# Kernel optimization log

Measured on AMD Instinct MI355X. Metric: run time of the kernel, lower is better.

The kernel has to match this reference:

```python
import jax, jax.numpy as jnp
import numpy as np

DIM = 640
M_SPATIAL = 100  # 10*10
BATCH = 64
EPS = 1e-5


def setup_inputs() -> dict:
    key = jax.random.key(0)
    kx, = jax.random.split(key, 1)
    x = jax.random.normal(kx, (BATCH, DIM, M_SPATIAL), dtype=jnp.float32)
    # temperature buffer: log(1 / (2 * H * W)) as in BDC.__init__
    t = jnp.log(1.0 / (2.0 * M_SPATIAL) * jnp.ones((1, 1), dtype=jnp.float32))
    return {"x": x, "t": t}


def reference(x, t):
    B, dim, M = x.shape
    # x_pow2 = x @ x^T  -> [B, dim, dim]
    x_pow2 = jnp.einsum('bim,bjm->bij', x, x)
    # I_M.bmm(x_pow2*I) broadcasts diag along rows; (x_pow2*I).bmm(I_M) along cols
    d = jnp.diagonal(x_pow2, axis1=1, axis2=2)  # [B, dim], squared norms
    dcov = d[:, :, None] + d[:, None, :] - 2.0 * x_pow2
    dcov = jnp.clip(dcov, 0.0)
    dcov = jnp.exp(t) * dcov
    dcov = jnp.sqrt(dcov + EPS)
    # double centering: dcov.bmm(I_M) = row sums broadcast, I_M.bmm(dcov) = col sums
    row_mean = jnp.sum(dcov, axis=2, keepdims=True) / dim          # [B, dim, 1]
    col_mean = jnp.sum(dcov, axis=1, keepdims=True) / dim          # [B, 1, dim]
    grand_mean = jnp.sum(dcov, axis=(1, 2), keepdims=True) / (dim * dim)
    bdc = dcov - row_mean - col_mean + grand_mean                   # [B, dim, dim]
    # Triuvec: upper triangle incl. diagonal, row-major order
    iu_r, iu_c = np.triu_indices(dim)
    return bdc[:, iu_r, iu_c]  # [B, dim*(dim+1)//2]
```

## Files before the change

### kernel.cpp

```cpp
#include <hip/hip_runtime.h>
#include <math.h>

#define BATCH 64
#define DIM   640
#define MSP   100
#define BT    128
#define NT2   5
#define NPAIR2 15
#define NBLK2 960
#define PTRI  205120
#define EPSV  1e-5f

#define WS_D 0
#define WS_S 40960
#define WS_G 81920
#define XB_OFF 327936ull

typedef __attribute__((ext_vector_type(8))) short short8;
typedef __attribute__((ext_vector_type(4))) float f32x4;

__device__ __forceinline__ short f2bf(float f) {
    union { float f; unsigned u; } x; x.f = f;
    unsigned r = x.u + 0x7fffu + ((x.u >> 16) & 1u);
    return (short)(r >> 16);
}
__device__ __forceinline__ float bf2f(short h) {
    union { unsigned u; float f; } x; x.u = ((unsigned)(unsigned short)h) << 16;
    return x.f;
}

__device__ __forceinline__ void decode_pair5(int u, int& ti, int& tj) {
    ti = 0;
    while (u >= NT2 - ti) { u -= NT2 - ti; ++ti; }
    tj = ti + u;
}

__device__ __forceinline__ void decode_block128(int bid, int& b, int& ti, int& tj) {
    const int xcd = bid & 7;
    const int idx = bid >> 3;
    b = xcd + 8 * (idx & 7);
    decode_pair5(idx >> 3, ti, tj);
}

__global__ __launch_bounds__(256) void k_prep(const float* __restrict__ x,
                                              float* __restrict__ ws) {
    short* xb = (short*)((char*)ws + XB_OFF);
    const int t = threadIdx.x;
    const int rr = t >> 4, c = t & 15;
    const int row = blockIdx.x * 16 + rr;
    const int k0 = c * 8;
    const float* src = x + (size_t)row * MSP;

    float v[8];
#pragma unroll
    for (int e = 0; e < 8; ++e) v[e] = 0.f;
    if (k0 <= 88) {
        float4 u0 = *(const float4*)(src + k0);
        float4 u1 = *(const float4*)(src + k0 + 4);
        v[0] = u0.x; v[1] = u0.y; v[2] = u0.z; v[3] = u0.w;
        v[4] = u1.x; v[5] = u1.y; v[6] = u1.z; v[7] = u1.w;
    } else if (k0 == 96) {
        float4 u0 = *(const float4*)(src + 96);
        v[0] = u0.x; v[1] = u0.y; v[2] = u0.z; v[3] = u0.w;
    }

    short8 h; float s = 0.f;
#pragma unroll
    for (int e = 0; e < 8; ++e) {
        short hb = f2bf(v[e]);
        float vr = bf2f(hb);
        s += vr * vr;
        h[e] = hb;
    }
    *(short8*)(xb + (size_t)blockIdx.x * 2048 + c * 128 + rr * 8) = h;

    s += __shfl_xor(s, 1); s += __shfl_xor(s, 2);
    s += __shfl_xor(s, 4); s += __shfl_xor(s, 8);
    if (c == 0) { ws[WS_D + row] = s; ws[WS_S + row] = 0.f; }
    if (blockIdx.x == 0 && t < BATCH) ws[WS_G + t] = 0.f;
}

__global__ __launch_bounds__(256) void k_sums(const float* __restrict__ tsc,
                                              float* __restrict__ ws) {
    __shared__ float sRow[BT];
    __shared__ float sCol[BT];

    int b, ti, tj;
    decode_block128(blockIdx.x, b, ti, tj);
    const int i0 = ti * BT, j0 = tj * BT;
    const int tid = threadIdx.x;
    const short* xb = (const short*)((const char*)ws + XB_OFF);

    if (tid < BT) { sRow[tid] = 0.f; sCol[tid] = 0.f; }

    const int wave = tid >> 6, lane = tid & 63;
    const int lm = lane & 15, lq = lane >> 4;
    const int r0 = (wave >> 1) * 64, c0 = (wave & 1) * 64;

    const short* pa = xb + (size_t)(b * 40 + ((i0 + r0) >> 4)) * 2048 + lq * 128 + lm * 8;
    const short* pb = xb + (size_t)(b * 40 + ((j0 + c0) >> 4)) * 2048 + lq * 128 + lm * 8;

    f32x4 acc[4][4] = {};
#pragma unroll
    for (int ks = 0; ks < 4; ++ks) {
        short8 af[4], bf[4];
#pragma unroll
        for (int m = 0; m < 4; ++m) af[m] = *(const short8*)(pa + m * 2048 + ks * 512);
#pragma unroll
        for (int n = 0; n < 4; ++n) bf[n] = *(const short8*)(pb + n * 2048 + ks * 512);
#pragma unroll
        for (int m = 0; m < 4; ++m)
#pragma unroll
            for (int n = 0; n < 4; ++n)
                acc[m][n] = __builtin_amdgcn_mfma_f32_16x16x32_bf16(af[m], bf[n], acc[m][n], 0, 0, 0);
    }

    const float scale = expf(tsc[0]);
    const float* dn = ws + WS_D + b * DIM;
    float dj[4];
#pragma unroll
    for (int n = 0; n < 4; ++n) dj[n] = dn[j0 + c0 + 16 * n + lm];

    float rp[4][4] = {}, cp[4] = {};
#pragma unroll
    for (int m = 0; m < 4; ++m) {
        float di_[4];
#pragma unroll
        for (int r = 0; r < 4; ++r) di_[r] = dn[i0 + r0 + 16 * m + 4 * lq + r];
#pragma unroll
        for (int n = 0; n < 4; ++n)
#pragma unroll
            for (int p = 0; p < 4; ++p) {
                float v = __builtin_amdgcn_sqrtf(
                    fmaf(scale, fmaxf(fmaf(-2.f, acc[m][n][p], di_[p] + dj[n]), 0.f), EPSV));
                rp[m][p] += v; cp[n] += v;
            }
    }

    __syncthreads();
#pragma unroll
    for (int m = 0; m < 4; ++m)
#pragma unroll
        for (int p = 0; p < 4; ++p) {
            float v = rp[m][p];
            v += __shfl_xor(v, 1); v += __shfl_xor(v, 2);
            v += __shfl_xor(v, 4); v += __shfl_xor(v, 8);
            if (lm == 0) atomicAdd(&sRow[r0 + 16 * m + 4 * lq + p], v);
        }
#pragma unroll
    for (int n = 0; n < 4; ++n) {
        float v = cp[n];
        v += __shfl_xor(v, 16); v += __shfl_xor(v, 32);
        if (lq == 0) atomicAdd(&sCol[c0 + 16 * n + lm], v);
    }
    __syncthreads();

    float* S = ws + WS_S + b * DIM;
    if (tid < BT) {
        atomicAdd(&S[i0 + tid], sRow[tid]);
        if (ti != tj) atomicAdd(&S[j0 + tid], sCol[tid]);
        float gg = sRow[tid];
        gg += __shfl_xor(gg, 1);  gg += __shfl_xor(gg, 2);  gg += __shfl_xor(gg, 4);
        gg += __shfl_xor(gg, 8);  gg += __shfl_xor(gg, 16); gg += __shfl_xor(gg, 32);
        if (lane == 0) atomicAdd(&ws[WS_G + b], (ti == tj ? 1.f : 2.f) * gg);
    }
}

__global__ __launch_bounds__(256) void k_write(const float* __restrict__ tsc,
                                               const float* __restrict__ ws,
                                               float* __restrict__ out) {
    int b, ti, tj;
    decode_block128(blockIdx.x, b, ti, tj);
    const int i0 = ti * BT, j0 = tj * BT;
    const int tid = threadIdx.x;
    const short* xb = (const short*)((const char*)ws + XB_OFF);

    const int wave = tid >> 6, lane = tid & 63;
    const int lm = lane & 15, lq = lane >> 4;
    const int wr = wave >> 1, wc = wave & 1;
    const int r0 = wr * 64, c0 = wc * 64;

    const bool diag = (ti == tj);
    if (diag && wr > wc) return;
    const bool pred = diag && (wr == wc);

    const short* pa = xb + (size_t)(b * 40 + ((i0 + r0) >> 4)) * 2048 + lq * 128 + lm * 8;
    const short* pb = xb + (size_t)(b * 40 + ((j0 + c0) >> 4)) * 2048 + lq * 128 + lm * 8;

    f32x4 acc[4][4] = {};
#pragma unroll
    for (int ks = 0; ks < 4; ++ks) {
        short8 af[4], bf[4];
#pragma unroll
        for (int m = 0; m < 4; ++m) af[m] = *(const short8*)(pa + m * 2048 + ks * 512);
#pragma unroll
        for (int n = 0; n < 4; ++n) bf[n] = *(const short8*)(pb + n * 2048 + ks * 512);
#pragma unroll
        for (int m = 0; m < 4; ++m)
#pragma unroll
            for (int n = 0; n < 4; ++n)
                acc[m][n] = __builtin_amdgcn_mfma_f32_16x16x32_bf16(af[m], bf[n], acc[m][n], 0, 0, 0);
    }

    const float scale = expf(tsc[0]);
    const float inv = 1.f / (float)DIM;
    const float gmean = ws[WS_G + b] * (inv * inv);
    const float* S  = ws + WS_S + b * DIM;
    const float* dn = ws + WS_D + b * DIM;

    float dj[4], bj[4]; int jj[4];
#pragma unroll
    for (int n = 0; n < 4; ++n) {
        int j = j0 + c0 + 16 * n + lm;
        jj[n] = j; dj[n] = dn[j]; bj[n] = -S[j] * inv;
    }

    float* outb = out + (size_t)b * PTRI;
#pragma unroll
    for (int m = 0; m < 4; ++m) {
        const int ibase = i0 + r0 + 16 * m + 4 * lq;
        float di_[4], ai_[4]; int ib_[4];
#pragma unroll
        for (int r = 0; r < 4; ++r) {
            int i = ibase + r;
            di_[r] = dn[i];
            ai_[r] = gmean - S[i] * inv;
            ib_[r] = i * DIM - (i * (i - 1)) / 2 - i;
        }
#pragma unroll
        for (int n = 0; n < 4; ++n)
#pragma unroll
            for (int p = 0; p < 4; ++p) {
                float v = __builtin_amdgcn_sqrtf(
                    fmaf(scale, fmaxf(fmaf(-2.f, acc[m][n][p], di_[p] + dj[n]), 0.f), EPSV));
                if (!pred || jj[n] >= ibase + p)
                    outb[ib_[p] + jj[n]] = v + ai_[p] + bj[n];
            }
    }
}

extern "C" void kernel_launch(void* const* d_in, const int* in_sizes, int n_in,
                              void* d_out, int out_size, void* d_ws, size_t ws_size,
                              hipStream_t stream) {
    const float* x = (const float*)d_in[0];
    const float* t = (const float*)d_in[1];
    float* out = (float*)d_out;
    float* ws  = (float*)d_ws;

    k_prep <<<dim3(BATCH * DIM / 16), 256, 0, stream>>>(x, ws);
    k_sums <<<dim3(NBLK2),            256, 0, stream>>>(t, ws);
    k_write<<<dim3(NBLK2),            256, 0, stream>>>(t, ws, out);
}
```

Measured before the change: 124.5 us.

## Fuse sums and write kernels with per-batch spin barrier, reusing MFMA results

Merges the row/column-sum kernel and the output-write kernel into one kernel. Each block keeps its Gram-tile accumulators and finishes the per-batch sums, then waits on a per-batch atomic counter until all 15 tile blocks of that batch have contributed. It then writes the centered output directly from registers, so the second bf16 GEMM pass and one kernel launch are no longer needed. The cost is spin-waiting and higher register pressure. Correctness relies on all 15 blocks of a batch being co-resident, which the launch bound of 4 blocks per CU and the block ordering are meant to guarantee.

```diff
diff --git a/kernel.cpp b/kernel.cpp
--- a/kernel.cpp
+++ b/kernel.cpp
@@ -14,7 +14,8 @@
 #define WS_D 0
 #define WS_S 40960
 #define WS_G 81920
-#define XB_OFF 327936ull
+#define WS_C 81984
+#define XB_OFF 328192ull
 
 typedef __attribute__((ext_vector_type(8))) short short8;
 typedef __attribute__((ext_vector_type(4))) float f32x4;
@@ -77,11 +78,15 @@
     s += __shfl_xor(s, 1); s += __shfl_xor(s, 2);
     s += __shfl_xor(s, 4); s += __shfl_xor(s, 8);
     if (c == 0) { ws[WS_D + row] = s; ws[WS_S + row] = 0.f; }
-    if (blockIdx.x == 0 && t < BATCH) ws[WS_G + t] = 0.f;
-}
-
-__global__ __launch_bounds__(256) void k_sums(const float* __restrict__ tsc,
-                                              float* __restrict__ ws) {
+    if (blockIdx.x == 0 && t < BATCH) {
+        ws[WS_G + t] = 0.f;
+        ((unsigned*)(ws + WS_C))[t] = 0u;
+    }
+}
+
+__global__ __launch_bounds__(256, 4) void k_main(const float* __restrict__ tsc,
+                                                 float* __restrict__ ws,
+                                                 float* __restrict__ out) {
     __shared__ float sRow[BT];
     __shared__ float sCol[BT];
 
@@ -95,7 +100,8 @@
 
     const int wave = tid >> 6, lane = tid & 63;
     const int lm = lane & 15, lq = lane >> 4;
-    const int r0 = (wave >> 1) * 64, c0 = (wave & 1) * 64;
+    const int wr = wave >> 1, wc = wave & 1;
+    const int r0 = wr * 64, c0 = wc * 64;
 
     const short* pa = xb + (size_t)(b * 40 + ((i0 + r0) >> 4)) * 2048 + lq * 128 + lm * 8;
     const short* pb = xb + (size_t)(b * 40 + ((j0 + c0) >> 4)) * 2048 + lq * 128 + lm * 8;
@@ -164,55 +170,35 @@
         gg += __shfl_xor(gg, 8);  gg += __shfl_xor(gg, 16); gg += __shfl_xor(gg, 32);
         if (lane == 0) atomicAdd(&ws[WS_G + b], (ti == tj ? 1.f : 2.f) * gg);
     }
-}
-
-__global__ __launch_bounds__(256) void k_write(const float* __restrict__ tsc,
-                                               const float* __restrict__ ws,
-                                               float* __restrict__ out) {
-    int b, ti, tj;
-    decode_block128(blockIdx.x, b, ti, tj);
-    const int i0 = ti * BT, j0 = tj * BT;
-    const int tid = threadIdx.x;
-    const short* xb = (const short*)((const char*)ws + XB_OFF);
-
-    const int wave = tid >> 6, lane = tid & 63;
-    const int lm = lane & 15, lq = lane >> 4;
-    const int wr = wave >> 1, wc = wave & 1;
-    const int r0 = wr * 64, c0 = wc * 64;
+
+    unsigned* cnt = (unsigned*)(ws + WS_C);
+    __threadfence();
+    __syncthreads();
+    if (tid == 0)
+        __hip_atomic_fetch_add(cnt + b, 1u, __ATOMIC_RELEASE,
+                               __HIP_MEMORY_SCOPE_AGENT);
+    if (tid == 0) {
+        while (__hip_atomic_load(cnt + b, __ATOMIC_ACQUIRE,
+                                 __HIP_MEMORY_SCOPE_AGENT) < (unsigned)NPAIR2)
+            __builtin_amdgcn_s_sleep(2);
+    }
+    __syncthreads();
 
     const bool diag = (ti == tj);
     if (diag && wr > wc) return;
     const bool pred = diag && (wr == wc);
 
-    const short* pa = xb + (size_t)(b * 40 + ((i0 + r0) >> 4)) * 2048 + lq * 128 + lm * 8;
-    const short* pb = xb + (size_t)(b * 40 + ((j0 + c0) >> 4)) * 2048 + lq * 128 + lm * 8;
-
-    f32x4 acc[4][4] = {};
-#pragma unroll
-    for (int ks = 0; ks < 4; ++ks) {
-        short8 af[4], bf[4];
-#pragma unroll
-        for (int m = 0; m < 4; ++m) af[m] = *(const short8*)(pa + m * 2048 + ks * 512);
-#pragma unroll
-        for (int n = 0; n < 4; ++n) bf[n] = *(const short8*)(pb + n * 2048 + ks * 512);
-#pragma unroll
-        for (int m = 0; m < 4; ++m)
-#pragma unroll
-            for (int n = 0; n < 4; ++n)
-                acc[m][n] = __builtin_amdgcn_mfma_f32_16x16x32_bf16(af[m], bf[n], acc[m][n], 0, 0, 0);
-    }
-
-    const float scale = expf(tsc[0]);
     const float inv = 1.f / (float)DIM;
-    const float gmean = ws[WS_G + b] * (inv * inv);
-    const float* S  = ws + WS_S + b * DIM;
-    const float* dn = ws + WS_D + b * DIM;
-
-    float dj[4], bj[4]; int jj[4];
+    const float gmean = __hip_atomic_load(ws + WS_G + b, __ATOMIC_RELAXED,
+                                          __HIP_MEMORY_SCOPE_AGENT) * (inv * inv);
+
+    float bj[4]; int jj[4];
 #pragma unroll
     for (int n = 0; n < 4; ++n) {
         int j = j0 + c0 + 16 * n + lm;
-        jj[n] = j; dj[n] = dn[j]; bj[n] = -S[j] * inv;
+        jj[n] = j;
+        bj[n] = -__hip_atomic_load(&S[j], __ATOMIC_RELAXED,
+                                   __HIP_MEMORY_SCOPE_AGENT) * inv;
     }
 
     float* outb = out + (size_t)b * PTRI;
@@ -224,7 +210,8 @@
         for (int r = 0; r < 4; ++r) {
             int i = ibase + r;
             di_[r] = dn[i];
-            ai_[r] = gmean - S[i] * inv;
+            ai_[r] = gmean - __hip_atomic_load(&S[i], __ATOMIC_RELAXED,
+                                               __HIP_MEMORY_SCOPE_AGENT) * inv;
             ib_[r] = i * DIM - (i * (i - 1)) / 2 - i;
         }
 #pragma unroll
@@ -247,7 +234,6 @@
     float* out = (float*)d_out;
     float* ws  = (float*)d_ws;
 
-    k_prep <<<dim3(BATCH * DIM / 16), 256, 0, stream>>>(x, ws);
-    k_sums <<<dim3(NBLK2),            256, 0, stream>>>(t, ws);
-    k_write<<<dim3(NBLK2),            256, 0, stream>>>(t, ws, out);
-}
+    k_prep<<<dim3(BATCH * DIM / 16), 256, 0, stream>>>(x, ws);
+    k_main<<<dim3(NBLK2),            256, 0, stream>>>(t, ws, out);
+}
```

Measured after the change: 278.9 us. 124% more time.
